# Kernel tuning notes

Measured on AMD Instinct MI355X. Metric: run time of the kernel, lower is better.

Reference implementation:

```python
import jax, jax.numpy as jnp
import numpy as np

N = 50000
E = 800000
EPS = 1e-16
NEG_SLOPE = 0.2

def setup_inputs() -> dict:
    key = jax.random.key(0)
    ks = jax.random.split(key, 10)
    s = lambda fan: 1.0 / np.sqrt(fan)
    return {
        "x": jax.random.normal(ks[0], (N, 128), dtype=jnp.float32),
        "edge_index": jax.random.randint(ks[1], (2, E), 0, N, dtype=jnp.int64),
        "W1": jax.random.normal(ks[2], (128, 4 * 32), dtype=jnp.float32) * s(128),
        "att_src1": jax.random.normal(ks[3], (4, 32), dtype=jnp.float32) * s(32),
        "att_dst1": jax.random.normal(ks[4], (4, 32), dtype=jnp.float32) * s(32),
        "b1": jnp.zeros((128,), dtype=jnp.float32),
        "W2": jax.random.normal(ks[5], (128, 2), dtype=jnp.float32) * s(128),
        "att_src2": jax.random.normal(ks[6], (1, 2), dtype=jnp.float32) * s(2),
        "att_dst2": jax.random.normal(ks[7], (1, 2), dtype=jnp.float32) * s(2),
        "b2": jnp.zeros((2,), dtype=jnp.float32),
    }

def _gat_conv(x, src, dst, W, att_src, att_dst, bias, heads, out_ch, concat):
    n = x.shape[0]
    h = (x @ W).reshape(n, heads, out_ch)                      # [N,H,C]
    a_src = jnp.sum(h * att_src[None], axis=-1)                # [N,H]
    a_dst = jnp.sum(h * att_dst[None], axis=-1)                # [N,H]
    e = jax.nn.leaky_relu(a_src[src] + a_dst[dst], NEG_SLOPE)  # [Etot,H]
    # segment softmax over incoming edges per destination node
    m = jax.ops.segment_max(e, dst, num_segments=n)            # [N,H]
    m = jnp.where(jnp.isfinite(m), m, 0.0)
    ex = jnp.exp(e - m[dst])
    denom = jax.ops.segment_sum(ex, dst, num_segments=n)       # [N,H]
    alpha = ex / (denom[dst] + EPS)                            # [Etot,H]
    out = jax.ops.segment_sum(alpha[:, :, None] * h[src], dst, num_segments=n)  # [N,H,C]
    if concat:
        out = out.reshape(n, heads * out_ch)
    else:
        out = out.mean(axis=1)
    return out + bias

def reference(x, edge_index, W1, att_src1, att_dst1, b1, W2, att_src2, att_dst2, b2):
    n = x.shape[0]
    # PyG GATConv adds self-loops by default
    loops = jnp.arange(n, dtype=edge_index.dtype)
    src = jnp.concatenate([edge_index[0], loops])
    dst = jnp.concatenate([edge_index[1], loops])
    # dropout is identity at inference
    h = jax.nn.elu(_gat_conv(x, src, dst, W1, att_src1, att_dst1, b1, 4, 32, True))
    h = _gat_conv(h, src, dst, W2, att_src2, att_dst2, b2, 1, 2, False)
    return jax.nn.log_softmax(h, axis=1)
```

## Files before the change

### kernel.cpp

```cpp
#include <hip/hip_runtime.h>
#include <hip/hip_bf16.h>

#define NN 50000
#define EE 800000
#define ET (EE + NN)
#define CAP 64
#define NEG_SLOPE 0.2f
#define EPSF 1e-16f
#define BUILD_BLOCKS 4096
#define GEMM_BLOCKS ((NN + 63) / 64)

typedef unsigned int uint32;
typedef __attribute__((ext_vector_type(8))) short short8;
typedef __attribute__((ext_vector_type(4))) float floatx4;

__device__ __forceinline__ unsigned short f2bf(float f) {
  unsigned int u = __float_as_uint(f);
  unsigned int r = (u + 0x7fffu + ((u >> 16) & 1u)) >> 16;
  return (unsigned short)r;
}
__device__ __forceinline__ float bf_lo(uint32 v) { return __uint_as_float(v << 16); }
__device__ __forceinline__ float bf_hi(uint32 v) { return __uint_as_float(v & 0xffff0000u); }


__device__ __forceinline__ void do_build(int b, int nb, const int* __restrict__ ei,
                                         int* __restrict__ counts,
                                         int* __restrict__ csr) {
  const int range = b & 7;
  const int lo = range * (NN / 8);
  const int hi = lo + (NN / 8);
  const int group = b >> 3;
  const int ngr = nb >> 3;
  for (int i = group * 256 + threadIdx.x; i < ET; i += ngr * 256) {
    int d = (i < EE) ? ei[EE + i] : (i - EE);
    if (d >= lo && d < hi) {
      int s = (i < EE) ? ei[i] : d;
      int r = atomicAdd(&counts[d], 1);
      if (r < CAP) csr[d * CAP + r] = s;
    }
  }
}

__device__ __forceinline__ void do_gemm_tile(
    int tile, const float* __restrict__ x, const unsigned short* __restrict__ Wt,
    const float* __restrict__ att_src1, const float* __restrict__ att_dst1,
    uint32* __restrict__ h1b, float* __restrict__ as1, float* __restrict__ ad1) {
  const int t    = threadIdx.x;
  const int wave = t >> 6;
  const int lane = t & 63;
  const int quad = lane >> 4;
  const int col  = lane & 15;
  const int nodeBase = tile * 64 + wave * 16;

  floatx4 acc[8];
  #pragma unroll
  for (int i = 0; i < 8; i++) acc[i] = (floatx4){0.f, 0.f, 0.f, 0.f};

  int mread = nodeBase + col; if (mread >= NN) mread = NN - 1;
  const float* __restrict__ xrow = x + (size_t)mread * 128 + quad * 8;
  const unsigned short* __restrict__ bbase = Wt + col * 128 + quad * 8;

  #pragma unroll
  for (int ks = 0; ks < 4; ks++) {
    float4 a0 = *(const float4*)(xrow + ks * 32);
    float4 a1 = *(const float4*)(xrow + ks * 32 + 4);
    union { short8 v; unsigned short u[8]; } af;
    af.u[0] = f2bf(a0.x); af.u[1] = f2bf(a0.y);
    af.u[2] = f2bf(a0.z); af.u[3] = f2bf(a0.w);
    af.u[4] = f2bf(a1.x); af.u[5] = f2bf(a1.y);
    af.u[6] = f2bf(a1.z); af.u[7] = f2bf(a1.w);
    #pragma unroll
    for (int tt = 0; tt < 8; tt++) {
      short8 bf = *(const short8*)(bbase + tt * 16 * 128 + ks * 32);
      acc[tt] = __builtin_amdgcn_mfma_f32_16x16x32_bf16(af.v, bf, acc[tt], 0, 0, 0);
    }
  }

  float asv[8], adv[8];
  #pragma unroll
  for (int tt = 0; tt < 8; tt++) {
    asv[tt] = att_src1[tt * 16 + col];
    adv[tt] = att_dst1[tt * 16 + col];
  }

  #pragma unroll
  for (int r = 0; r < 4; r++) {
    const int gn = nodeBase + quad * 4 + r;
    const bool live = (gn < NN);
    #pragma unroll
    for (int tt = 0; tt < 8; tt++) {
      float v = acc[tt][r];
      float w = __shfl_xor(v, 1, 64);
      if (live && ((col & 1) == 0)) {
        uint32 pk = (uint32)f2bf(v) | ((uint32)f2bf(w) << 16);
        h1b[(size_t)gn * 64 + tt * 8 + (col >> 1)] = pk;
      }
    }
    #pragma unroll
    for (int h = 0; h < 4; h++) {
      float ps = acc[2 * h][r] * asv[2 * h] + acc[2 * h + 1][r] * asv[2 * h + 1];
      float pd = acc[2 * h][r] * adv[2 * h] + acc[2 * h + 1][r] * adv[2 * h + 1];
      #pragma unroll
      for (int off = 1; off < 16; off <<= 1) {
        ps += __shfl_xor(ps, off, 64);
        pd += __shfl_xor(pd, off, 64);
      }
      if (live && col == 0) {
        as1[gn * 4 + h] = ps;
        ad1[gn * 4 + h] = pd;
      }
    }
  }
}

__device__ __forceinline__ void do_agg1_group(
    int g, const int* __restrict__ counts, const int* __restrict__ csr,
    const uint32* __restrict__ h1b, const float* __restrict__ as1,
    const float* __restrict__ ad1, const float* __restrict__ b1,
    const float* __restrict__ W2, const float* __restrict__ att_src2,
    const float* __restrict__ att_dst2,
    float* __restrict__ h2, float* __restrict__ as2, float* __restrict__ ad2) {
  const int lane = threadIdx.x & 63;
  const int wv = threadIdx.x >> 6;
  const int hd = lane >> 4;
  const int n = __builtin_amdgcn_readfirstlane(g * 4 + wv);

  const int cnt = __builtin_amdgcn_readfirstlane(counts[n]);
  const int* __restrict__ row = csr + n * CAP;
  const float adv = ad1[n * 4 + hd];

  float den = 0.f, accx = 0.f, accy = 0.f;
  int j = 0;
  for (; j + 3 < cnt; j += 4) {
    int s0 = row[j], s1 = row[j + 1], s2 = row[j + 2], s3 = row[j + 3];
    float e0 = as1[s0 * 4 + hd] + adv;
    float e1 = as1[s1 * 4 + hd] + adv;
    float e2 = as1[s2 * 4 + hd] + adv;
    float e3 = as1[s3 * 4 + hd] + adv;
    uint32 v0 = h1b[s0 * 64 + lane];
    uint32 v1 = h1b[s1 * 64 + lane];
    uint32 v2 = h1b[s2 * 64 + lane];
    uint32 v3 = h1b[s3 * 64 + lane];
    e0 = (e0 > 0.f) ? e0 : NEG_SLOPE * e0;
    e1 = (e1 > 0.f) ? e1 : NEG_SLOPE * e1;
    e2 = (e2 > 0.f) ? e2 : NEG_SLOPE * e2;
    e3 = (e3 > 0.f) ? e3 : NEG_SLOPE * e3;
    float x0 = __expf(e0), x1 = __expf(e1), x2 = __expf(e2), x3 = __expf(e3);
    den += (x0 + x1) + (x2 + x3);
    accx = fmaf(x0, bf_lo(v0), accx);
    accy = fmaf(x0, bf_hi(v0), accy);
    accx = fmaf(x1, bf_lo(v1), accx);
    accy = fmaf(x1, bf_hi(v1), accy);
    accx = fmaf(x2, bf_lo(v2), accx);
    accy = fmaf(x2, bf_hi(v2), accy);
    accx = fmaf(x3, bf_lo(v3), accx);
    accy = fmaf(x3, bf_hi(v3), accy);
  }
  for (; j < cnt; j++) {
    int s = row[j];
    float e = as1[s * 4 + hd] + adv;
    e = (e > 0.f) ? e : NEG_SLOPE * e;
    float ex = __expf(e);
    uint32 v = h1b[s * 64 + lane];
    den += ex;
    accx = fmaf(ex, bf_lo(v), accx);
    accy = fmaf(ex, bf_hi(v), accy);
  }

  float inv = 1.f / (den + EPSF);
  float2 bb = ((const float2*)b1)[lane];
  float ox = accx * inv + bb.x;
  float oy = accy * inv + bb.y;
  ox = (ox > 0.f) ? ox : (__expf(ox) - 1.f);
  oy = (oy > 0.f) ? oy : (__expf(oy) - 1.f);

  float4 wq = ((const float4*)W2)[lane];
  float p0 = ox * wq.x + oy * wq.z;
  float p1 = ox * wq.y + oy * wq.w;
  #pragma unroll
  for (int off = 32; off; off >>= 1) {
    p0 += __shfl_xor(p0, off, 64);
    p1 += __shfl_xor(p1, off, 64);
  }
  if (lane == 0) {
    *(float2*)&h2[n * 2] = make_float2(p0, p1);
    as2[n] = p0 * att_src2[0] + p1 * att_src2[1];
    ad2[n] = p0 * att_dst2[0] + p1 * att_dst2[1];
  }
}

__device__ __forceinline__ void do_agg2_item(
    int i, const int* __restrict__ counts, const int* __restrict__ csr,
    const float* __restrict__ h2, const float* __restrict__ as2,
    const float* __restrict__ ad2, const float* __restrict__ b2,
    float* __restrict__ out) {
  int n = i >> 3;
  int sub = i & 7;
  const float adv = ad2[n];
  const int cnt = counts[n];
  const int* __restrict__ row = csr + n * CAP;
  const float2* __restrict__ h2v = (const float2*)h2;

  float den = 0.f, a0 = 0.f, a1 = 0.f;
  for (int j = sub; j < cnt; j += 8) {
    int s = row[j];
    float e = as2[s] + adv;
    e = (e > 0.f) ? e : NEG_SLOPE * e;
    float ex = __expf(e);
    float2 hv = h2v[s];
    den += ex;
    a0 = fmaf(ex, hv.x, a0);
    a1 = fmaf(ex, hv.y, a1);
  }
  #pragma unroll
  for (int off = 4; off; off >>= 1) {
    den += __shfl_down(den, off, 8);
    a0  += __shfl_down(a0, off, 8);
    a1  += __shfl_down(a1, off, 8);
  }
  if (sub == 0) {
    float inv = 1.f / (den + EPSF);
    float o0 = a0 * inv + b2[0];
    float o1 = a1 * inv + b2[1];
    float mx = fmaxf(o0, o1);
    float lse = mx + __logf(__expf(o0 - mx) + __expf(o1 - mx));
    *(float2*)&out[n * 2] = make_float2(o0 - lse, o1 - lse);
  }
}

__global__ __launch_bounds__(256) void prep_zero_k(
    const float* __restrict__ W1, unsigned short* __restrict__ Wt,
    int* __restrict__ counts) {
  const int step = gridDim.x * 256;
  for (int i = blockIdx.x * 256 + threadIdx.x; i < NN; i += step) counts[i] = 0;
  for (int i = blockIdx.x * 256 + threadIdx.x; i < 128 * 128; i += step) {
    int k = i >> 7, c = i & 127;
    Wt[c * 128 + k] = f2bf(W1[i]);
  }
}

__global__ __launch_bounds__(256) void work_k(
    const int* __restrict__ ei, int* __restrict__ counts, int* __restrict__ csr,
    const float* __restrict__ x, const unsigned short* __restrict__ Wt,
    const float* __restrict__ att_src1, const float* __restrict__ att_dst1,
    uint32* __restrict__ h1b, float* __restrict__ as1, float* __restrict__ ad1) {
  const int b = blockIdx.x;
  if (b < BUILD_BLOCKS) {
    do_build(b, BUILD_BLOCKS, ei, counts, csr);
  } else {
    do_gemm_tile(b - BUILD_BLOCKS, x, Wt, att_src1, att_dst1, h1b, as1, ad1);
  }
}

__global__ __launch_bounds__(256) void agg1_k(
    const int* __restrict__ counts, const int* __restrict__ csr,
    const uint32* __restrict__ h1b, const float* __restrict__ as1,
    const float* __restrict__ ad1, const float* __restrict__ b1,
    const float* __restrict__ W2, const float* __restrict__ att_src2,
    const float* __restrict__ att_dst2,
    float* __restrict__ h2, float* __restrict__ as2, float* __restrict__ ad2) {
  do_agg1_group(blockIdx.x, counts, csr, h1b, as1, ad1, b1, W2,
                att_src2, att_dst2, h2, as2, ad2);
}

__global__ __launch_bounds__(256) void agg2_k(
    const int* __restrict__ counts, const int* __restrict__ csr,
    const float* __restrict__ h2, const float* __restrict__ as2,
    const float* __restrict__ ad2, const float* __restrict__ b2,
    float* __restrict__ out) {
  int i = blockIdx.x * 256 + threadIdx.x;
  if (i < NN * 8) do_agg2_item(i, counts, csr, h2, as2, ad2, b2, out);
}

extern "C" void kernel_launch(void* const* d_in, const int* in_sizes, int n_in,
                              void* d_out, int out_size, void* d_ws, size_t ws_size,
                              hipStream_t stream) {
  const float* x        = (const float*)d_in[0];
  const int*   ei       = (const int*)d_in[1];
  const float* W1       = (const float*)d_in[2];
  const float* att_src1 = (const float*)d_in[3];
  const float* att_dst1 = (const float*)d_in[4];
  const float* b1       = (const float*)d_in[5];
  const float* W2       = (const float*)d_in[6];
  const float* att_src2 = (const float*)d_in[7];
  const float* att_dst2 = (const float*)d_in[8];
  const float* b2       = (const float*)d_in[9];
  float* out = (float*)d_out;

  char* p = (char*)d_ws;
  auto alloc = [&](size_t bytes) {
    char* r = p;
    p += (bytes + 255) & ~size_t(255);
    return r;
  };
  uint32* h1b  = (uint32*)alloc(sizeof(uint32) * NN * 64);
  float* as1   = (float*)alloc(sizeof(float) * NN * 4);
  float* ad1   = (float*)alloc(sizeof(float) * NN * 4);
  float* h2    = (float*)alloc(sizeof(float) * NN * 2);
  float* as2   = (float*)alloc(sizeof(float) * NN);
  float* ad2   = (float*)alloc(sizeof(float) * NN);
  int*   counts = (int*)alloc(sizeof(int) * NN);
  int*   csr   = (int*)alloc(sizeof(int) * NN * CAP);
  unsigned short* Wt = (unsigned short*)alloc(sizeof(unsigned short) * 128 * 128);

  prep_zero_k<<<256, 256, 0, stream>>>(W1, Wt, counts);
  work_k<<<BUILD_BLOCKS + GEMM_BLOCKS, 256, 0, stream>>>(
      ei, counts, csr, x, Wt, att_src1, att_dst1, h1b, as1, ad1);
  agg1_k<<<NN / 4, 256, 0, stream>>>(counts, csr, h1b, as1, ad1, b1, W2,
                                     att_src2, att_dst2, h2, as2, ad2);
  agg2_k<<<(NN * 8 + 255) / 256, 256, 0, stream>>>(counts, csr, h2, as2, ad2,
                                                   b2, out);
}
```

Baseline: 195.2 us.

## Pad atomic counters, pre-seed self-loops, split agg1 edges across two waves, pack layer-2 record

The CSR build now spaces each node's counter 16 ints apart to cut atomic contention on shared cache lines. Self-loops are written directly into the first CSR slot with the count starting at 1, and edges are read two at a time as int2 pairs. Layer-1 aggregation splits each node's edge list between two waves, which are combined through shared memory, to raise parallelism per node. Layer-2 features and attention scalars are packed into one float4 record per node so each neighbour needs a single gather. The costs are a 16x larger counter array to zero and a block-wide barrier in agg1.

```diff
diff --git a/kernel.cpp b/kernel.cpp
--- a/kernel.cpp
+++ b/kernel.cpp
@@ -3,12 +3,13 @@
 
 #define NN 50000
 #define EE 800000
-#define ET (EE + NN)
 #define CAP 64
+#define CSTRIDE 16
 #define NEG_SLOPE 0.2f
 #define EPSF 1e-16f
 #define BUILD_BLOCKS 4096
 #define GEMM_BLOCKS ((NN + 63) / 64)
+#define NPAIRS (EE / 2)
 
 typedef unsigned int uint32;
 typedef __attribute__((ext_vector_type(8))) short short8;
@@ -22,21 +23,33 @@
 __device__ __forceinline__ float bf_lo(uint32 v) { return __uint_as_float(v << 16); }
 __device__ __forceinline__ float bf_hi(uint32 v) { return __uint_as_float(v & 0xffff0000u); }
 
-
-__device__ __forceinline__ void do_build(int b, int nb, const int* __restrict__ ei,
+__device__ __forceinline__ void do_build(int b, const int* __restrict__ ei,
                                          int* __restrict__ counts,
                                          int* __restrict__ csr) {
   const int range = b & 7;
   const int lo = range * (NN / 8);
   const int hi = lo + (NN / 8);
   const int group = b >> 3;
-  const int ngr = nb >> 3;
-  for (int i = group * 256 + threadIdx.x; i < ET; i += ngr * 256) {
-    int d = (i < EE) ? ei[EE + i] : (i - EE);
-    if (d >= lo && d < hi) {
-      int s = (i < EE) ? ei[i] : d;
-      int r = atomicAdd(&counts[d], 1);
-      if (r < CAP) csr[d * CAP + r] = s;
+  const int tid0 = group * 256 + threadIdx.x;
+  const int stride = (BUILD_BLOCKS >> 3) * 256;
+
+  {
+    int n = lo + tid0;
+    if (n < hi) csr[n * CAP] = n;
+  }
+
+  const int2* __restrict__ dst2 = (const int2*)(ei + EE);
+  const int2* __restrict__ src2 = (const int2*)(ei);
+  for (int p = tid0; p < NPAIRS; p += stride) {
+    int2 d2 = dst2[p];
+    int2 s2 = src2[p];
+    if (d2.x >= lo && d2.x < hi) {
+      int r = atomicAdd(&counts[d2.x * CSTRIDE], 1);
+      if (r < CAP) csr[d2.x * CAP + r] = s2.x;
+    }
+    if (d2.y >= lo && d2.y < hi) {
+      int r = atomicAdd(&counts[d2.y * CSTRIDE], 1);
+      if (r < CAP) csr[d2.y * CAP + r] = s2.y;
     }
   }
 }
@@ -113,25 +126,57 @@
   }
 }
 
-__device__ __forceinline__ void do_agg1_group(
-    int g, const int* __restrict__ counts, const int* __restrict__ csr,
+__global__ __launch_bounds__(256) void prep_zero_k(
+    const float* __restrict__ W1, unsigned short* __restrict__ Wt,
+    int* __restrict__ counts) {
+  const int step = gridDim.x * 256;
+  const int t0 = blockIdx.x * 256 + threadIdx.x;
+  for (int i = t0; i < NN * CSTRIDE; i += step)
+    counts[i] = ((i & (CSTRIDE - 1)) == 0) ? 1 : 0;
+  for (int i = t0; i < 128 * 128; i += step) {
+    int k = i >> 7, c = i & 127;
+    Wt[c * 128 + k] = f2bf(W1[i]);
+  }
+}
+
+__global__ __launch_bounds__(256) void work_k(
+    const int* __restrict__ ei, int* __restrict__ counts, int* __restrict__ csr,
+    const float* __restrict__ x, const unsigned short* __restrict__ Wt,
+    const float* __restrict__ att_src1, const float* __restrict__ att_dst1,
+    uint32* __restrict__ h1b, float* __restrict__ as1, float* __restrict__ ad1) {
+  const int b = blockIdx.x;
+  if (b < BUILD_BLOCKS) {
+    do_build(b, ei, counts, csr);
+  } else {
+    do_gemm_tile(b - BUILD_BLOCKS, x, Wt, att_src1, att_dst1, h1b, as1, ad1);
+  }
+}
+
+__global__ __launch_bounds__(256) void agg1_k(
+    const int* __restrict__ counts, const int* __restrict__ csr,
     const uint32* __restrict__ h1b, const float* __restrict__ as1,
     const float* __restrict__ ad1, const float* __restrict__ b1,
     const float* __restrict__ W2, const float* __restrict__ att_src2,
-    const float* __restrict__ att_dst2,
-    float* __restrict__ h2, float* __restrict__ as2, float* __restrict__ ad2) {
+    const float* __restrict__ att_dst2, float4* __restrict__ rec) {
+  __shared__ float part[2][3][64];
   const int lane = threadIdx.x & 63;
-  const int wv = threadIdx.x >> 6;
-  const int hd = lane >> 4;
-  const int n = __builtin_amdgcn_readfirstlane(g * 4 + wv);
-
-  const int cnt = __builtin_amdgcn_readfirstlane(counts[n]);
+  const int wv   = threadIdx.x >> 6;
+  const int nl   = wv >> 1;
+  const int w    = wv & 1;
+  const int hd   = lane >> 4;
+  const int n = __builtin_amdgcn_readfirstlane(blockIdx.x * 2 + nl);
+
+  int cnt = counts[n * CSTRIDE];
+  cnt = __builtin_amdgcn_readfirstlane(cnt < CAP ? cnt : CAP);
+  const int half = (cnt + 1) >> 1;
+  const int jbeg = w ? half : 0;
+  const int jend = w ? cnt : half;
   const int* __restrict__ row = csr + n * CAP;
   const float adv = ad1[n * 4 + hd];
 
   float den = 0.f, accx = 0.f, accy = 0.f;
-  int j = 0;
-  for (; j + 3 < cnt; j += 4) {
+  int j = jbeg;
+  for (; j + 3 < jend; j += 4) {
     int s0 = row[j], s1 = row[j + 1], s2 = row[j + 2], s3 = row[j + 3];
     float e0 = as1[s0 * 4 + hd] + adv;
     float e1 = as1[s1 * 4 + hd] + adv;
@@ -156,7 +201,7 @@
     accx = fmaf(x3, bf_lo(v3), accx);
     accy = fmaf(x3, bf_hi(v3), accy);
   }
-  for (; j < cnt; j++) {
+  for (; j < jend; j++) {
     int s = row[j];
     float e = as1[s * 4 + hd] + adv;
     e = (e > 0.f) ? e : NEG_SLOPE * e;
@@ -167,6 +212,17 @@
     accy = fmaf(ex, bf_hi(v), accy);
   }
 
+  if (w == 1) {
+    part[nl][0][lane] = den;
+    part[nl][1][lane] = accx;
+    part[nl][2][lane] = accy;
+  }
+  __syncthreads();
+  if (w == 1) return;
+  den  += part[nl][0][lane];
+  accx += part[nl][1][lane];
+  accy += part[nl][2][lane];
+
   float inv = 1.f / (den + EPSF);
   float2 bb = ((const float2*)b1)[lane];
   float ox = accx * inv + bb.x;
@@ -183,34 +239,35 @@
     p1 += __shfl_xor(p1, off, 64);
   }
   if (lane == 0) {
-    *(float2*)&h2[n * 2] = make_float2(p0, p1);
-    as2[n] = p0 * att_src2[0] + p1 * att_src2[1];
-    ad2[n] = p0 * att_dst2[0] + p1 * att_dst2[1];
-  }
-}
-
-__device__ __forceinline__ void do_agg2_item(
-    int i, const int* __restrict__ counts, const int* __restrict__ csr,
-    const float* __restrict__ h2, const float* __restrict__ as2,
-    const float* __restrict__ ad2, const float* __restrict__ b2,
+    rec[n] = make_float4(p0, p1,
+                         p0 * att_src2[0] + p1 * att_src2[1],
+                         p0 * att_dst2[0] + p1 * att_dst2[1]);
+  }
+}
+
+__global__ __launch_bounds__(256) void agg2_k(
+    const int* __restrict__ counts, const int* __restrict__ csr,
+    const float4* __restrict__ rec, const float* __restrict__ b2,
     float* __restrict__ out) {
+  int i = blockIdx.x * 256 + threadIdx.x;
+  if (i >= NN * 8) return;
   int n = i >> 3;
   int sub = i & 7;
-  const float adv = ad2[n];
-  const int cnt = counts[n];
+  const float adv = rec[n].w;
+  int cnt = counts[n * CSTRIDE];
+  cnt = cnt < CAP ? cnt : CAP;
   const int* __restrict__ row = csr + n * CAP;
-  const float2* __restrict__ h2v = (const float2*)h2;
 
   float den = 0.f, a0 = 0.f, a1 = 0.f;
   for (int j = sub; j < cnt; j += 8) {
     int s = row[j];
-    float e = as2[s] + adv;
+    float4 rs = rec[s];
+    float e = rs.z + adv;
     e = (e > 0.f) ? e : NEG_SLOPE * e;
     float ex = __expf(e);
-    float2 hv = h2v[s];
     den += ex;
-    a0 = fmaf(ex, hv.x, a0);
-    a1 = fmaf(ex, hv.y, a1);
+    a0 = fmaf(ex, rs.x, a0);
+    a1 = fmaf(ex, rs.y, a1);
   }
   #pragma unroll
   for (int off = 4; off; off >>= 1) {
@@ -226,50 +283,6 @@
     float lse = mx + __logf(__expf(o0 - mx) + __expf(o1 - mx));
     *(float2*)&out[n * 2] = make_float2(o0 - lse, o1 - lse);
   }
-}
-
-__global__ __launch_bounds__(256) void prep_zero_k(
-    const float* __restrict__ W1, unsigned short* __restrict__ Wt,
-    int* __restrict__ counts) {
-  const int step = gridDim.x * 256;
-  for (int i = blockIdx.x * 256 + threadIdx.x; i < NN; i += step) counts[i] = 0;
-  for (int i = blockIdx.x * 256 + threadIdx.x; i < 128 * 128; i += step) {
-    int k = i >> 7, c = i & 127;
-    Wt[c * 128 + k] = f2bf(W1[i]);
-  }
-}
-
-__global__ __launch_bounds__(256) void work_k(
-    const int* __restrict__ ei, int* __restrict__ counts, int* __restrict__ csr,
-    const float* __restrict__ x, const unsigned short* __restrict__ Wt,
-    const float* __restrict__ att_src1, const float* __restrict__ att_dst1,
-    uint32* __restrict__ h1b, float* __restrict__ as1, float* __restrict__ ad1) {
-  const int b = blockIdx.x;
-  if (b < BUILD_BLOCKS) {
-    do_build(b, BUILD_BLOCKS, ei, counts, csr);
-  } else {
-    do_gemm_tile(b - BUILD_BLOCKS, x, Wt, att_src1, att_dst1, h1b, as1, ad1);
-  }
-}
-
-__global__ __launch_bounds__(256) void agg1_k(
-    const int* __restrict__ counts, const int* __restrict__ csr,
-    const uint32* __restrict__ h1b, const float* __restrict__ as1,
-    const float* __restrict__ ad1, const float* __restrict__ b1,
-    const float* __restrict__ W2, const float* __restrict__ att_src2,
-    const float* __restrict__ att_dst2,
-    float* __restrict__ h2, float* __restrict__ as2, float* __restrict__ ad2) {
-  do_agg1_group(blockIdx.x, counts, csr, h1b, as1, ad1, b1, W2,
-                att_src2, att_dst2, h2, as2, ad2);
-}
-
-__global__ __launch_bounds__(256) void agg2_k(
-    const int* __restrict__ counts, const int* __restrict__ csr,
-    const float* __restrict__ h2, const float* __restrict__ as2,
-    const float* __restrict__ ad2, const float* __restrict__ b2,
-    float* __restrict__ out) {
-  int i = blockIdx.x * 256 + threadIdx.x;
-  if (i < NN * 8) do_agg2_item(i, counts, csr, h2, as2, ad2, b2, out);
 }
 
 extern "C" void kernel_launch(void* const* d_in, const int* in_sizes, int n_in,
@@ -296,18 +309,15 @@
   uint32* h1b  = (uint32*)alloc(sizeof(uint32) * NN * 64);
   float* as1   = (float*)alloc(sizeof(float) * NN * 4);
   float* ad1   = (float*)alloc(sizeof(float) * NN * 4);
-  float* h2    = (float*)alloc(sizeof(float) * NN * 2);
-  float* as2   = (float*)alloc(sizeof(float) * NN);
-  float* ad2   = (float*)alloc(sizeof(float) * NN);
-  int*   counts = (int*)alloc(sizeof(int) * NN);
+  float4* rec  = (float4*)alloc(sizeof(float4) * NN);
+  int*   counts = (int*)alloc(sizeof(int) * NN * CSTRIDE);
   int*   csr   = (int*)alloc(sizeof(int) * NN * CAP);
   unsigned short* Wt = (unsigned short*)alloc(sizeof(unsigned short) * 128 * 128);
 
-  prep_zero_k<<<256, 256, 0, stream>>>(W1, Wt, counts);
+  prep_zero_k<<<512, 256, 0, stream>>>(W1, Wt, counts);
   work_k<<<BUILD_BLOCKS + GEMM_BLOCKS, 256, 0, stream>>>(
       ei, counts, csr, x, Wt, att_src1, att_dst1, h1b, as1, ad1);
-  agg1_k<<<NN / 4, 256, 0, stream>>>(counts, csr, h1b, as1, ad1, b1, W2,
-                                     att_src2, att_dst2, h2, as2, ad2);
-  agg2_k<<<(NN * 8 + 255) / 256, 256, 0, stream>>>(counts, csr, h2, as2, ad2,
-                                                   b2, out);
-}
+  agg1_k<<<NN / 2, 256, 0, stream>>>(counts, csr, h1b, as1, ad1, b1, W2,
+                                     att_src2, att_dst2, rec);
+  agg2_k<<<(NN * 8 + 255) / 256, 256, 0, stream>>>(counts, csr, rec, b2, out);
+}
```

Result: slower. 208.1 us (+6.6%).
